# Kernel tuning notes

Hardware: AMD Instinct MI355X
Metric: run time of the kernel (lower is better)

## Reference

```python
import jax, jax.numpy as jnp
import numpy as np

D_MODEL = 1024
NUM_HEADS = 16
HEAD_DIM = D_MODEL // NUM_HEADS


def setup_inputs() -> dict:
    key = jax.random.key(0)
    ks = jax.random.split(key, 10)
    B, SQ, SKV = 4, 2048, 2048
    s = 1.0 / np.sqrt(D_MODEL)
    return {
        "query": jax.random.normal(ks[0], (B, SQ, D_MODEL), jnp.float32),
        "key_value": jax.random.normal(ks[1], (B, SKV, D_MODEL), jnp.float32),
        "Wq": jax.random.normal(ks[2], (D_MODEL, D_MODEL), jnp.float32) * s,
        "bq": jnp.zeros((D_MODEL,), jnp.float32),
        "Wk": jax.random.normal(ks[3], (D_MODEL, D_MODEL), jnp.float32) * s,
        "bk": jnp.zeros((D_MODEL,), jnp.float32),
        "Wv": jax.random.normal(ks[4], (D_MODEL, D_MODEL), jnp.float32) * s,
        "bv": jnp.zeros((D_MODEL,), jnp.float32),
        "Wo": jax.random.normal(ks[5], (D_MODEL, D_MODEL), jnp.float32) * s,
        "bo": jnp.zeros((D_MODEL,), jnp.float32),
    }


def reference(query, key_value, Wq, bq, Wk, bk, Wv, bv, Wo, bo):
    B, SQ, _ = query.shape
    SKV = key_value.shape[1]
    H, Dh = NUM_HEADS, HEAD_DIM
    # projections (torch Linear: x @ W.T + b); split heads -> (B, H, S, Dh)
    Q = (query @ Wq.T + bq).reshape(B, SQ, H, Dh).transpose(0, 2, 1, 3)
    K = (key_value @ Wk.T + bk).reshape(B, SKV, H, Dh).transpose(0, 2, 1, 3)
    V = (key_value @ Wv.T + bv).reshape(B, SKV, H, Dh).transpose(0, 2, 1, 3)
    scale = jnp.asarray(np.sqrt(Dh), query.dtype)
    scores = jnp.einsum("bhqd,bhkd->bhqk", Q, K) / scale
    weights = jax.nn.softmax(scores, axis=-1)  # dropout is identity in eval
    attn = jnp.einsum("bhqk,bhkd->bhqd", weights, V)
    attn = attn.transpose(0, 2, 1, 3).reshape(B, SQ, H * Dh)
    return attn @ Wo.T + bo
```

## Files before the change

kernel.cpp:

```cpp
#include <hip/hip_runtime.h>

#define NH 16
#define DH 64
#define DM 1024
#define SEQ 2048
#define BATCH 4

typedef short s16x8 __attribute__((ext_vector_type(8)));
typedef float f32x4 __attribute__((ext_vector_type(4)));

__device__ __forceinline__ unsigned short f2bf(float f) {
  union { float f; unsigned int u; } v; v.f = f;
  unsigned int u = v.u;
  unsigned int r = (u + 0x7fffu + ((u >> 16) & 1u)) >> 16;
  return (unsigned short)r;
}

__device__ __forceinline__ unsigned int pkbf(float a, float b) {
#if __has_builtin(__builtin_amdgcn_cvt_pk_bf16_f32)
  typedef short v2s __attribute__((ext_vector_type(2)));
  v2s r = __builtin_amdgcn_cvt_pk_bf16_f32(a, b);
  union { v2s v; unsigned int u; } cv; cv.v = r;
  return cv.u;
#else
  return (unsigned int)f2bf(a) | ((unsigned int)f2bf(b) << 16);
#endif
}

__device__ __forceinline__ float fexp2(float x) {
#if __has_builtin(__builtin_amdgcn_exp2f)
  return __builtin_amdgcn_exp2f(x);
#else
  return exp2f(x);
#endif
}

__device__ __forceinline__ void gload_lds16(const void* g, void* l) {
  __builtin_amdgcn_global_load_lds(
      (const __attribute__((address_space(1))) unsigned int*)g,
      (__attribute__((address_space(3))) unsigned int*)l, 16, 0, 0);
}

__global__ void convert_all(const float* __restrict__ q, const float* __restrict__ kv,
                            const float* __restrict__ w0, const float* __restrict__ w1,
                            const float* __restrict__ w2, const float* __restrict__ w3,
                            unsigned short* __restrict__ oq, unsigned short* __restrict__ okv,
                            unsigned short* __restrict__ ow0, unsigned short* __restrict__ ow1,
                            unsigned short* __restrict__ ow2, unsigned short* __restrict__ ow3) {
  const int NQ4 = (BATCH * SEQ * DM) / 4;
  const int NW4 = (DM * DM) / 4;
  const int total = NQ4 * 2 + NW4 * 4;
  for (int i = blockIdx.x * blockDim.x + threadIdx.x; i < total;
       i += gridDim.x * blockDim.x) {
    const float* s; unsigned short* d; int off;
    if (i < NQ4)            { s = q;  d = oq;  off = i; }
    else if (i < 2 * NQ4)   { s = kv; d = okv; off = i - NQ4; }
    else {
      int j = i - 2 * NQ4; int wsel = j / NW4; off = j - wsel * NW4;
      s = (wsel == 0) ? w0 : (wsel == 1) ? w1 : (wsel == 2) ? w2 : w3;
      d = (wsel == 0) ? ow0 : (wsel == 1) ? ow1 : (wsel == 2) ? ow2 : ow3;
    }
    float4 v = *(const float4*)(s + (size_t)off * 4);
    ushort4 o;
    o.x = f2bf(v.x); o.y = f2bf(v.y); o.z = f2bf(v.z); o.w = f2bf(v.w);
    *(ushort4*)(d + (size_t)off * 4) = o;
  }
}

__device__ __forceinline__ void gemm_tile(const unsigned short* __restrict__ X,
                                          const unsigned short* __restrict__ Wt,
                                          unsigned short* As, unsigned short* Bs,
                                          int m0, int n0, f32x4 (*acc)[4]) {
  const int tid = threadIdx.x;
  const int wv_ = tid >> 6, lane = tid & 63;
  const int quad = lane >> 4, c = lane & 15;
  const int wm = (wv_ >> 1) * 64, wn = (wv_ & 1) * 64;
  const int srow = lane >> 3;
  const int scol = ((lane & 7) ^ srow) * 8;

  for (int kt = 0; kt < DM; kt += 64) {
#pragma unroll
    for (int i = 0; i < 4; ++i) {
      int reg = wv_ * 4 + i;
      gload_lds16(X + (size_t)(m0 + reg * 8 + srow) * DM + kt + scol,
                  (void*)(As + reg * 512));
      gload_lds16(Wt + (size_t)(n0 + reg * 8 + srow) * DM + kt + scol,
                  (void*)(Bs + reg * 512));
    }
    __syncthreads();
#pragma unroll
    for (int k2 = 0; k2 < 2; ++k2) {
      s16x8 a[4], b[4];
      int g = k2 * 4 + quad;
#pragma unroll
      for (int t = 0; t < 4; ++t)
        a[t] = *(const s16x8*)(As + (wm + t * 16 + c) * 64 + ((g ^ (c & 7)) * 8));
#pragma unroll
      for (int t = 0; t < 4; ++t)
        b[t] = *(const s16x8*)(Bs + (wn + t * 16 + c) * 64 + ((g ^ (c & 7)) * 8));
#pragma unroll
      for (int tm = 0; tm < 4; ++tm)
#pragma unroll
        for (int tn = 0; tn < 4; ++tn)
          acc[tm][tn] = __builtin_amdgcn_mfma_f32_16x16x32_bf16(
              a[tm], b[tn], acc[tm][tn], 0, 0, 0);
    }
    __syncthreads();
  }
}

__global__ __launch_bounds__(256)
void gemm_qkv(const unsigned short* __restrict__ Xq,
              const unsigned short* __restrict__ Xkv,
              const unsigned short* __restrict__ W0,
              const unsigned short* __restrict__ W1,
              const unsigned short* __restrict__ W2,
              const float* __restrict__ b0, const float* __restrict__ b1,
              const float* __restrict__ b2,
              unsigned short* __restrict__ OQ, unsigned short* __restrict__ OK_,
              unsigned short* __restrict__ OV) {
  __shared__ alignas(16) unsigned short As[128 * 64];
  __shared__ alignas(16) unsigned short Bs[128 * 64];
  const int m0 = blockIdx.x * 128;
  const int ysel = blockIdx.y >> 3;
  const int n0 = (blockIdx.y & 7) * 128;
  const unsigned short* X = (ysel == 0) ? Xq : Xkv;
  const unsigned short* Wt = (ysel == 0) ? W0 : (ysel == 1) ? W1 : W2;
  const float* bias = (ysel == 0) ? b0 : (ysel == 1) ? b1 : b2;
  unsigned short* Out = (ysel == 0) ? OQ : (ysel == 1) ? OK_ : OV;
  const float scale = (ysel == 0) ? 0.1803368801f : 1.0f;

  f32x4 acc[4][4] = {};
  gemm_tile(X, Wt, As, Bs, m0, n0, acc);

  const int tid = threadIdx.x;
  const int wv_ = tid >> 6, lane = tid & 63;
  const int quad = lane >> 4, c = lane & 15;
  const int wm = (wv_ >> 1) * 64, wn = (wv_ & 1) * 64;
#pragma unroll
  for (int tm = 0; tm < 4; ++tm) {
#pragma unroll
    for (int tn = 0; tn < 4; ++tn) {
      int n = n0 + wn + tn * 16 + c;
      float bv = bias[n];
      int m_base = m0 + wm + tm * 16 + quad * 4;
      if (ysel == 2) {
        int b_ = m_base >> 11, s_ = m_base & 2047, h_ = n >> 6, dh = n & 63;
        size_t idx = (((size_t)(b_ * NH + h_)) * DH + dh) * SEQ + s_;
        ushort4 o4;
        o4.x = f2bf(acc[tm][tn][0] + bv);
        o4.y = f2bf(acc[tm][tn][1] + bv);
        o4.z = f2bf(acc[tm][tn][2] + bv);
        o4.w = f2bf(acc[tm][tn][3] + bv);
        *(ushort4*)(&Out[idx]) = o4;
      } else {
#pragma unroll
        for (int p = 0; p < 4; ++p) {
          int m = m_base + p;
          float val = (acc[tm][tn][p] + bv) * scale;
          int b_ = m >> 11, s_ = m & 2047, h_ = n >> 6, dh = n & 63;
          size_t idx = (((size_t)(b_ * NH + h_)) * SEQ + s_) * DH + dh;
          Out[idx] = f2bf(val);
        }
      }
    }
  }
}

__global__ __launch_bounds__(256)
void gemm_o(const unsigned short* __restrict__ X,
            const unsigned short* __restrict__ Wt,
            const float* __restrict__ bias, float* __restrict__ Out) {
  __shared__ alignas(16) unsigned short As[128 * 64];
  __shared__ alignas(16) unsigned short Bs[128 * 64];
  const int m0 = blockIdx.x * 128;
  const int n0 = blockIdx.y * 128;
  f32x4 acc[4][4] = {};
  gemm_tile(X, Wt, As, Bs, m0, n0, acc);

  const int tid = threadIdx.x;
  const int wv_ = tid >> 6, lane = tid & 63;
  const int quad = lane >> 4, c = lane & 15;
  const int wm = (wv_ >> 1) * 64, wn = (wv_ & 1) * 64;
#pragma unroll
  for (int tm = 0; tm < 4; ++tm) {
#pragma unroll
    for (int tn = 0; tn < 4; ++tn) {
      int n = n0 + wn + tn * 16 + c;
      float bv = bias[n];
#pragma unroll
      for (int p = 0; p < 4; ++p) {
        int m = m0 + wm + tm * 16 + quad * 4 + p;
        Out[(size_t)m * DM + n] = acc[tm][tn][p] + bv;
      }
    }
  }
}

__global__ __launch_bounds__(512, 4)
void attn_kernel(const unsigned short* __restrict__ Qb,
                 const unsigned short* __restrict__ Kb,
                 const unsigned short* __restrict__ VTb,
                 unsigned short* __restrict__ Ob) {
  __shared__ alignas(16) unsigned short SM[18432];

  const int tid = threadIdx.x, wv_ = tid >> 6, lane = tid & 63;
  const int quad = lane >> 4, c = lane & 15;
  const int wg = blockIdx.x;
  const int bh = (wg & 7) + 8 * (wg >> 6);
  const int qb = (wg >> 3) & 7;
  const unsigned short* Qp = Qb + (size_t)bh * SEQ * DH;
  const unsigned short* Kp = Kb + (size_t)bh * SEQ * DH;
  const unsigned short* Vp = VTb + (size_t)bh * DH * SEQ;
  const int wq0 = qb * 256 + wv_ * 32;

  s16x8 aq[2][2];
#pragma unroll
  for (int t = 0; t < 2; ++t)
#pragma unroll
    for (int k2 = 0; k2 < 2; ++k2)
      aq[t][k2] = *(const s16x8*)(Qp + (size_t)(wq0 + t * 16 + c) * DH +
                                  k2 * 32 + quad * 8);

  f32x4 ot[4][2] = {};
  f32x4 lacc[2] = {};
  s16x8 ones;
  {
    union { s16x8 v; unsigned short u[8]; } o_;
#pragma unroll
    for (int j = 0; j < 8; ++j) o_.u[j] = 0x3F80;
    ones = o_.v;
  }

  const int srow = lane >> 3;
  const int sbase = (lane & 7) ^ (srow & 3);

  const int fK = (c & 3) | (((c >> 2) & 1) << 2);
  const int fV = (c & 3) | (((c >> 3) & 1) << 2);

#pragma unroll
  for (int i = 0; i < 2; ++i) {
    int slab = wv_ * 2 + i;
    if (slab < 8) {
      int ch = sbase ^ ((slab & 1) << 2);
      gload_lds16(Kp + (size_t)(slab * 8 + srow) * DH + ch * 8,
                  (void*)(SM + slab * 512));
    } else {
      int s2 = slab - 8;
      int ch = sbase ^ ((s2 & 1) << 2);
      gload_lds16(Vp + (size_t)(s2 * 8 + srow) * SEQ + ch * 8,
                  (void*)(SM + 8192 + s2 * 512));
    }
  }

  for (int kt = 0; kt < SEQ; kt += 64) {
    const int cur = (kt >> 6) & 1;
    __syncthreads();
    if (kt + 64 < SEQ) {
      const int nxt = cur ^ 1;
#pragma unroll
      for (int i = 0; i < 2; ++i) {
        int slab = wv_ * 2 + i;
        if (slab < 8) {
          int ch = sbase ^ ((slab & 1) << 2);
          gload_lds16(Kp + (size_t)(kt + 64 + slab * 8 + srow) * DH + ch * 8,
                      (void*)(SM + nxt * 4096 + slab * 512));
        } else {
          int s2 = slab - 8;
          int ch = sbase ^ ((s2 & 1) << 2);
          gload_lds16(Vp + (size_t)(s2 * 8 + srow) * SEQ + kt + 64 + ch * 8,
                      (void*)(SM + 8192 + nxt * 4096 + s2 * 512));
        }
      }
    }
    const unsigned short* K_ = SM + cur * 4096;
    const unsigned short* V_ = SM + 8192 + cur * 4096;

    f32x4 s[2][2][2] = {};
#pragma unroll
    for (int k2 = 0; k2 < 2; ++k2) {
      s16x8 ak[2][2];
#pragma unroll
      for (int jp = 0; jp < 2; ++jp)
#pragma unroll
        for (int h = 0; h < 2; ++h) {
          int r = jp * 32 + ((c >> 2) << 3) + h * 4 + (c & 3);
          int g = k2 * 4 + quad;
          ak[jp][h] = *(const s16x8*)(K_ + r * 64 + ((g ^ fK) * 8));
        }
#pragma unroll
      for (int t = 0; t < 2; ++t)
#pragma unroll
        for (int jp = 0; jp < 2; ++jp)
#pragma unroll
          for (int h = 0; h < 2; ++h)
            s[t][jp][h] = __builtin_amdgcn_mfma_f32_16x16x32_bf16(
                ak[jp][h], aq[t][k2], s[t][jp][h], 0, 0, 0);
    }

    s16x8 bp[2][2];
#pragma unroll
    for (int t = 0; t < 2; ++t)
#pragma unroll
      for (int jp = 0; jp < 2; ++jp) {
        float e00 = fexp2(s[t][jp][0][0]);
        float e01 = fexp2(s[t][jp][0][1]);
        float e02 = fexp2(s[t][jp][0][2]);
        float e03 = fexp2(s[t][jp][0][3]);
        float e10 = fexp2(s[t][jp][1][0]);
        float e11 = fexp2(s[t][jp][1][1]);
        float e12 = fexp2(s[t][jp][1][2]);
        float e13 = fexp2(s[t][jp][1][3]);
        union { s16x8 v; unsigned int u[4]; } pk;
        pk.u[0] = pkbf(e00, e01);
        pk.u[1] = pkbf(e02, e03);
        pk.u[2] = pkbf(e10, e11);
        pk.u[3] = pkbf(e12, e13);
        bp[t][jp] = pk.v;
        lacc[t] = __builtin_amdgcn_mfma_f32_16x16x32_bf16(
            ones, bp[t][jp], lacc[t], 0, 0, 0);
      }

#pragma unroll
    for (int jp = 0; jp < 2; ++jp)
#pragma unroll
      for (int dt = 0; dt < 4; ++dt) {
        int g = jp * 4 + quad;
        int r = dt * 16 + c;
        s16x8 av = *(const s16x8*)(V_ + r * 64 + ((g ^ fV) * 8));
#pragma unroll
        for (int t = 0; t < 2; ++t)
          ot[dt][t] = __builtin_amdgcn_mfma_f32_16x16x32_bf16(
              av, bp[t][jp], ot[dt][t], 0, 0, 0);
      }
  }

  __syncthreads();

  const int b_ = bh >> 4, h_ = bh & 15;
  const int ql = lane >> 1, hf = lane & 1;
  unsigned short* Lq = SM + wv_ * (32 * 72);
#pragma unroll
  for (int t = 0; t < 2; ++t) {
    float inv = 1.0f / lacc[t][0];
#pragma unroll
    for (int dt = 0; dt < 4; ++dt) {
      unsigned int w01 = pkbf(ot[dt][t][0] * inv, ot[dt][t][1] * inv);
      unsigned int w23 = pkbf(ot[dt][t][2] * inv, ot[dt][t][3] * inv);
      unsigned short* p = Lq + (t * 16 + c) * 72 + dt * 16 + quad * 4;
      *(unsigned int*)(p) = w01;
      *(unsigned int*)(p + 2) = w23;
    }
  }
  const unsigned short* Lr = Lq + ql * 72 + hf * 32;
  unsigned short* Og = Ob + ((size_t)(b_ * SEQ + wq0 + ql)) * DM + h_ * 64 + hf * 32;
#pragma unroll
  for (int j = 0; j < 4; ++j) {
    s16x8 v = *(const s16x8*)(Lr + j * 8);
    *(s16x8*)(Og + j * 8) = v;
  }
}

extern "C" void kernel_launch(void* const* d_in, const int* in_sizes, int n_in,
                              void* d_out, int out_size, void* d_ws, size_t ws_size,
                              hipStream_t stream) {
  const float* q  = (const float*)d_in[0];
  const float* kv = (const float*)d_in[1];
  const float* Wq = (const float*)d_in[2];
  const float* bq = (const float*)d_in[3];
  const float* Wk = (const float*)d_in[4];
  const float* bk = (const float*)d_in[5];
  const float* Wv = (const float*)d_in[6];
  const float* bv = (const float*)d_in[7];
  const float* Wo = (const float*)d_in[8];
  const float* bo = (const float*)d_in[9];

  char* ws = (char*)d_ws;
  const size_t MB = 1024 * 1024;
  unsigned short* q_bf  = (unsigned short*)(ws);
  unsigned short* kv_bf = (unsigned short*)(ws + 16 * MB);
  unsigned short* wq_bf = (unsigned short*)(ws + 32 * MB);
  unsigned short* wk_bf = (unsigned short*)(ws + 34 * MB);
  unsigned short* wv_bf = (unsigned short*)(ws + 36 * MB);
  unsigned short* wo_bf = (unsigned short*)(ws + 38 * MB);
  unsigned short* Qb    = (unsigned short*)(ws + 40 * MB);
  unsigned short* Kb    = (unsigned short*)(ws + 56 * MB);
  unsigned short* VTb   = (unsigned short*)(ws + 72 * MB);
  unsigned short* attn  = (unsigned short*)(ws + 88 * MB);

  convert_all<<<2048, 256, 0, stream>>>(q, kv, Wq, Wk, Wv, Wo,
                                        q_bf, kv_bf, wq_bf, wk_bf, wv_bf, wo_bf);
  gemm_qkv<<<dim3(64, 24), 256, 0, stream>>>(q_bf, kv_bf, wq_bf, wk_bf, wv_bf,
                                             bq, bk, bv, Qb, Kb, VTb);
  attn_kernel<<<dim3(512), 512, 0, stream>>>(Qb, Kb, VTb, attn);
  gemm_o<<<dim3(64, 8), 256, 0, stream>>>(attn, wo_bf, bo, (float*)d_out);
}
```

Before: 307.9 us.

## Switch attention inner loop from 16x16x32 to 32x32x16 bf16 MFMA tiles

Rewrites the attention kernel's QK^T, row-sum and PV matrix products to use 32x32x16 MFMA instructions instead of 16x16x32 ones. Each wave now handles its 32 query rows as a single tile, with new K/V LDS addressing and swizzle indices matched to the 32x32 operand layout, and a reworked epilogue. The aim is fewer MFMA issues and fewer LDS fragment loads per key block. The cost is larger accumulator register footprint and fresh index math that has to match the existing LDS swizzle.

```diff
diff --git a/kernel.cpp b/kernel.cpp
--- a/kernel.cpp
+++ b/kernel.cpp
@@ -8,6 +8,7 @@
 
 typedef short s16x8 __attribute__((ext_vector_type(8)));
 typedef float f32x4 __attribute__((ext_vector_type(4)));
+typedef float f32x16 __attribute__((ext_vector_type(16)));
 
 __device__ __forceinline__ unsigned short f2bf(float f) {
   union { float f; unsigned int u; } v; v.f = f;
@@ -205,7 +206,7 @@
   __shared__ alignas(16) unsigned short SM[18432];
 
   const int tid = threadIdx.x, wv_ = tid >> 6, lane = tid & 63;
-  const int quad = lane >> 4, c = lane & 15;
+  const int q31 = lane & 31, hi = lane >> 5;
   const int wg = blockIdx.x;
   const int bh = (wg & 7) + 8 * (wg >> 6);
   const int qb = (wg >> 3) & 7;
@@ -214,16 +215,13 @@
   const unsigned short* Vp = VTb + (size_t)bh * DH * SEQ;
   const int wq0 = qb * 256 + wv_ * 32;
 
-  s16x8 aq[2][2];
-#pragma unroll
-  for (int t = 0; t < 2; ++t)
-#pragma unroll
-    for (int k2 = 0; k2 < 2; ++k2)
-      aq[t][k2] = *(const s16x8*)(Qp + (size_t)(wq0 + t * 16 + c) * DH +
-                                  k2 * 32 + quad * 8);
-
-  f32x4 ot[4][2] = {};
-  f32x4 lacc[2] = {};
+  s16x8 aq[4];
+#pragma unroll
+  for (int d0 = 0; d0 < 4; ++d0)
+    aq[d0] = *(const s16x8*)(Qp + (size_t)(wq0 + q31) * DH + d0 * 16 + hi * 8);
+
+  f32x16 ot[2] = {};
+  f32x16 lacc = {};
   s16x8 ones;
   {
     union { s16x8 v; unsigned short u[8]; } o_;
@@ -235,8 +233,10 @@
   const int srow = lane >> 3;
   const int sbase = (lane & 7) ^ (srow & 3);
 
-  const int fK = (c & 3) | (((c >> 2) & 1) << 2);
-  const int fV = (c & 3) | (((c >> 3) & 1) << 2);
+  const int l7 = lane & 7;
+  const int fV = (lane & 3) | (((lane >> 3) & 1) << 2);
+  const int kR64 = ((lane & 3) | ((lane & 8) >> 1) | ((lane & 4) << 1) |
+                    (lane & 16)) * 64;
 
 #pragma unroll
   for (int i = 0; i < 2; ++i) {
@@ -276,82 +276,62 @@
     const unsigned short* K_ = SM + cur * 4096;
     const unsigned short* V_ = SM + 8192 + cur * 4096;
 
-    f32x4 s[2][2][2] = {};
-#pragma unroll
-    for (int k2 = 0; k2 < 2; ++k2) {
-      s16x8 ak[2][2];
-#pragma unroll
-      for (int jp = 0; jp < 2; ++jp)
-#pragma unroll
-        for (int h = 0; h < 2; ++h) {
-          int r = jp * 32 + ((c >> 2) << 3) + h * 4 + (c & 3);
-          int g = k2 * 4 + quad;
-          ak[jp][h] = *(const s16x8*)(K_ + r * 64 + ((g ^ fK) * 8));
-        }
-#pragma unroll
-      for (int t = 0; t < 2; ++t)
-#pragma unroll
-        for (int jp = 0; jp < 2; ++jp)
-#pragma unroll
-          for (int h = 0; h < 2; ++h)
-            s[t][jp][h] = __builtin_amdgcn_mfma_f32_16x16x32_bf16(
-                ak[jp][h], aq[t][k2], s[t][jp][h], 0, 0, 0);
-    }
-
-    s16x8 bp[2][2];
-#pragma unroll
-    for (int t = 0; t < 2; ++t)
-#pragma unroll
-      for (int jp = 0; jp < 2; ++jp) {
-        float e00 = fexp2(s[t][jp][0][0]);
-        float e01 = fexp2(s[t][jp][0][1]);
-        float e02 = fexp2(s[t][jp][0][2]);
-        float e03 = fexp2(s[t][jp][0][3]);
-        float e10 = fexp2(s[t][jp][1][0]);
-        float e11 = fexp2(s[t][jp][1][1]);
-        float e12 = fexp2(s[t][jp][1][2]);
-        float e13 = fexp2(s[t][jp][1][3]);
+#pragma unroll
+    for (int kb = 0; kb < 2; ++kb) {
+      f32x16 sa = {};
+#pragma unroll
+      for (int d0 = 0; d0 < 4; ++d0) {
+        s16x8 ak = *(const s16x8*)(K_ + kb * 2048 + kR64 +
+                                   (((d0 * 2 + hi) ^ l7) * 8));
+        sa = __builtin_amdgcn_mfma_f32_32x32x16_bf16(ak, aq[d0], sa, 0, 0, 0);
+      }
+
+      float e[16];
+#pragma unroll
+      for (int r = 0; r < 16; ++r) e[r] = fexp2(sa[r]);
+      s16x8 bp0, bp1;
+      {
         union { s16x8 v; unsigned int u[4]; } pk;
-        pk.u[0] = pkbf(e00, e01);
-        pk.u[1] = pkbf(e02, e03);
-        pk.u[2] = pkbf(e10, e11);
-        pk.u[3] = pkbf(e12, e13);
-        bp[t][jp] = pk.v;
-        lacc[t] = __builtin_amdgcn_mfma_f32_16x16x32_bf16(
-            ones, bp[t][jp], lacc[t], 0, 0, 0);
-      }
-
-#pragma unroll
-    for (int jp = 0; jp < 2; ++jp)
-#pragma unroll
-      for (int dt = 0; dt < 4; ++dt) {
-        int g = jp * 4 + quad;
-        int r = dt * 16 + c;
-        s16x8 av = *(const s16x8*)(V_ + r * 64 + ((g ^ fV) * 8));
-#pragma unroll
-        for (int t = 0; t < 2; ++t)
-          ot[dt][t] = __builtin_amdgcn_mfma_f32_16x16x32_bf16(
-              av, bp[t][jp], ot[dt][t], 0, 0, 0);
-      }
+        pk.u[0] = pkbf(e[0], e[1]);  pk.u[1] = pkbf(e[2], e[3]);
+        pk.u[2] = pkbf(e[4], e[5]);  pk.u[3] = pkbf(e[6], e[7]);
+        bp0 = pk.v;
+        pk.u[0] = pkbf(e[8], e[9]);  pk.u[1] = pkbf(e[10], e[11]);
+        pk.u[2] = pkbf(e[12], e[13]); pk.u[3] = pkbf(e[14], e[15]);
+        bp1 = pk.v;
+      }
+      lacc = __builtin_amdgcn_mfma_f32_32x32x16_bf16(ones, bp0, lacc, 0, 0, 0);
+      lacc = __builtin_amdgcn_mfma_f32_32x32x16_bf16(ones, bp1, lacc, 0, 0, 0);
+
+#pragma unroll
+      for (int dt = 0; dt < 2; ++dt) {
+        int row = dt * 32 + q31;
+        s16x8 av0 = *(const s16x8*)(V_ + row * 64 +
+                                    (((kb * 4 + hi) ^ fV) * 8));
+        ot[dt] = __builtin_amdgcn_mfma_f32_32x32x16_bf16(av0, bp0, ot[dt], 0, 0, 0);
+        s16x8 av1 = *(const s16x8*)(V_ + row * 64 +
+                                    (((kb * 4 + 2 + hi) ^ fV) * 8));
+        ot[dt] = __builtin_amdgcn_mfma_f32_32x32x16_bf16(av1, bp1, ot[dt], 0, 0, 0);
+      }
+    }
   }
 
   __syncthreads();
 
   const int b_ = bh >> 4, h_ = bh & 15;
-  const int ql = lane >> 1, hf = lane & 1;
+  const float inv = 1.0f / lacc[0];
   unsigned short* Lq = SM + wv_ * (32 * 72);
 #pragma unroll
-  for (int t = 0; t < 2; ++t) {
-    float inv = 1.0f / lacc[t][0];
-#pragma unroll
-    for (int dt = 0; dt < 4; ++dt) {
-      unsigned int w01 = pkbf(ot[dt][t][0] * inv, ot[dt][t][1] * inv);
-      unsigned int w23 = pkbf(ot[dt][t][2] * inv, ot[dt][t][3] * inv);
-      unsigned short* p = Lq + (t * 16 + c) * 72 + dt * 16 + quad * 4;
+  for (int dt = 0; dt < 2; ++dt) {
+#pragma unroll
+    for (int a = 0; a < 4; ++a) {
+      unsigned int w01 = pkbf(ot[dt][4 * a] * inv, ot[dt][4 * a + 1] * inv);
+      unsigned int w23 = pkbf(ot[dt][4 * a + 2] * inv, ot[dt][4 * a + 3] * inv);
+      unsigned short* p = Lq + q31 * 72 + dt * 32 + a * 8 + hi * 4;
       *(unsigned int*)(p) = w01;
       *(unsigned int*)(p + 2) = w23;
     }
   }
+  const int ql = lane >> 1, hf = lane & 1;
   const unsigned short* Lr = Lq + ql * 72 + hf * 32;
   unsigned short* Og = Ob + ((size_t)(b_ * SEQ + wq0 + ql)) * DM + h_ * 64 + hf * 32;
 #pragma unroll
```

New measurement: 321.6 us. 1.04x slower.
